# Kernel tuning notes

Hardware: AMD Instinct MI355X
Metric: run time of the kernel (lower is better)

## Reference

```python
import jax, jax.numpy as jnp
import numpy as np

L = 6          # n_layers
T = 256        # seq_len
B = 32         # batch
N = 1024       # n_features (factor_dim)
H = 16         # n_heads
HD = 64        # head_dim
PD = H * HD    # packed_dim_size == N here
FF = 4096      # dim_feedforward
EPS = 1e-5


def setup_inputs() -> dict:
    key = jax.random.key(0)
    ks = jax.random.split(key, 6)
    s = 0.02  # weight init scale (xavier-ish for these dims)
    return {
        "src": jax.random.normal(ks[0], (T, B, N), jnp.float32),
        "attn_mask": jnp.zeros((T, T), jnp.float32),  # additive mask
        "Wqkv": jax.random.normal(ks[1], (L, 3 * PD, N), jnp.float32) * s,
        "bqkv": jnp.zeros((L, 3 * PD), jnp.float32),
        "Wo": jax.random.normal(ks[2], (L, N, PD), jnp.float32) * s,
        "bo": jnp.zeros((L, N), jnp.float32),
        "ln1_g": jnp.ones((L, N), jnp.float32),
        "ln1_b": jnp.zeros((L, N), jnp.float32),
        "ln2_g": jnp.ones((L, N), jnp.float32),
        "ln2_b": jnp.zeros((L, N), jnp.float32),
        "W1": jax.random.normal(ks[3], (L, FF, N), jnp.float32) * s,
        "b1": jnp.zeros((L, FF), jnp.float32),
        "W2": jax.random.normal(ks[4], (L, N, FF), jnp.float32) * s,
        "b2": jnp.zeros((L, N), jnp.float32),
        "lnf_g": jnp.ones((N,), jnp.float32),
        "lnf_b": jnp.zeros((N,), jnp.float32),
    }


def _layer_norm(x, g, b):
    m = x.mean(-1, keepdims=True)
    v = ((x - m) ** 2).mean(-1, keepdims=True)
    return (x - m) * jax.lax.rsqrt(v + EPS) * g + b


def reference(src, attn_mask, Wqkv, bqkv, Wo, bo, ln1_g, ln1_b, ln2_g, ln2_b,
              W1, b1, W2, b2, lnf_g, lnf_b):
    inv_sqrt_hd = 1.0 / np.sqrt(HD).astype(np.float32)

    def layer(x, p):
        wqkv, bq, wo, bo_, g1, bb1n, g2, bb2n, w1, bb1, w2, bb2 = p
        # --- self-attention block (pre-norm) ---
        h = _layer_norm(x, g1, bb1n)                       # [T,B,N]
        qkv = jnp.einsum('tbn,pn->tbp', h, wqkv) + bq      # [T,B,3*PD]
        q, k, v = jnp.split(qkv, 3, axis=-1)
        q = q.reshape(T, B, H, HD) * inv_sqrt_hd
        k = k.reshape(T, B, H, HD)
        v = v.reshape(T, B, H, HD)
        scores = jnp.einsum('tbhd,sbhd->bhts', q, k) + attn_mask  # [B,H,T,T]
        probs = jax.nn.softmax(scores, axis=-1)
        o = jnp.einsum('bhts,sbhd->tbhd', probs, v).reshape(T, B, PD)
        x = x + jnp.einsum('tbp,np->tbn', o, wo) + bo_
        # --- FFN block (pre-norm) ---
        h = _layer_norm(x, g2, bb2n)
        ff = jax.nn.relu(jnp.einsum('tbn,fn->tbf', h, w1) + bb1)
        x = x + jnp.einsum('tbf,nf->tbn', ff, w2) + bb2
        return x, None

    params = (Wqkv, bqkv, Wo, bo, ln1_g, ln1_b, ln2_g, ln2_b, W1, b1, W2, b2)
    x, _ = jax.lax.scan(layer, src, params)
    return _layer_norm(x, lnf_g, lnf_b)
```

## Files before the change

### kernel.cpp

```cpp
#include <hip/hip_runtime.h>
#include <math.h>

#define TS 256
#define BS 32
#define NF 1024
#define NH 16
#define HD 64
#define PD 1024
#define FFD 4096
#define NLAYER 6
#define ROWS (TS*BS)
#define LNEPS 1e-5f

typedef unsigned int u32;
typedef __attribute__((ext_vector_type(8))) short bf16x8;
typedef __attribute__((ext_vector_type(4))) float f32x4;

__device__ __forceinline__ unsigned short f2bf(float f) {
    u32 u = __builtin_bit_cast(u32, f);
    u32 r = (u + 0x7fffu + ((u >> 16) & 1u)) >> 16;
    return (unsigned short)r;
}

__device__ __forceinline__ void async16(const void* g, void* l) {
    __builtin_amdgcn_global_load_lds(
        (const __attribute__((address_space(1))) u32*)g,
        (__attribute__((address_space(3))) u32*)l, 16, 0, 0);
}

template <int BF16OUT>
__global__ __launch_bounds__(256)
void ln_kernel(const float* __restrict__ x, void* __restrict__ y,
               const float* __restrict__ g, const float* __restrict__ b) {
    int row = blockIdx.x;
    int tid = threadIdx.x;
    const float4* xr = (const float4*)(x + (size_t)row * NF);
    float4 v = xr[tid];
    float s  = v.x + v.y + v.z + v.w;
    float ss = v.x*v.x + v.y*v.y + v.z*v.z + v.w*v.w;
    #pragma unroll
    for (int off = 32; off > 0; off >>= 1) {
        s  += __shfl_down(s,  off);
        ss += __shfl_down(ss, off);
    }
    __shared__ float ws[4], wss[4];
    int wid = tid >> 6, lane = tid & 63;
    if (lane == 0) { ws[wid] = s; wss[wid] = ss; }
    __syncthreads();
    float sum   = ws[0] + ws[1] + ws[2] + ws[3];
    float sumsq = wss[0] + wss[1] + wss[2] + wss[3];
    float mean = sum * (1.0f / NF);
    float var  = sumsq * (1.0f / NF) - mean * mean;
    float rstd = rsqrtf(var + LNEPS);
    float4 gv = ((const float4*)g)[tid];
    float4 bv = ((const float4*)b)[tid];
    float4 o;
    o.x = (v.x - mean) * rstd * gv.x + bv.x;
    o.y = (v.y - mean) * rstd * gv.y + bv.y;
    o.z = (v.z - mean) * rstd * gv.z + bv.z;
    o.w = (v.w - mean) * rstd * gv.w + bv.w;
    if (BF16OUT) {
        ushort4 ov;
        ov.x = f2bf(o.x); ov.y = f2bf(o.y); ov.z = f2bf(o.z); ov.w = f2bf(o.w);
        ((ushort4*)((unsigned short*)y + (size_t)row * NF))[tid] = ov;
    } else {
        ((float4*)((float*)y + (size_t)row * NF))[tid] = o;
    }
}

__global__ __launch_bounds__(256)
void f2bf4_kernel(const float* __restrict__ s0, const float* __restrict__ s1,
                  const float* __restrict__ s2, const float* __restrict__ s3,
                  unsigned short* __restrict__ d0, unsigned short* __restrict__ d1,
                  unsigned short* __restrict__ d2, unsigned short* __restrict__ d3,
                  int n0, int n1, int n2, int n3) {
    const float* s; unsigned short* d; int n;
    switch (blockIdx.y) {
        case 0: s = s0; d = d0; n = n0; break;
        case 1: s = s1; d = d1; n = n1; break;
        case 2: s = s2; d = d2; n = n2; break;
        default: s = s3; d = d3; n = n3; break;
    }
    int i = (blockIdx.x * 256 + threadIdx.x) * 4;
    if (i >= n) return;
    float4 v = *(const float4*)(s + i);
    ushort4 o;
    o.x = f2bf(v.x); o.y = f2bf(v.y); o.z = f2bf(v.z); o.w = f2bf(v.w);
    *(ushort4*)(d + i) = o;
}

template <int MODE, int RESID>
__global__ __launch_bounds__(256)
void gemm_mfma(const unsigned short* __restrict__ A, const unsigned short* __restrict__ B,
               const float* __restrict__ bias, const float* __restrict__ resid,
               void* __restrict__ Cout, int M, int N, int K) {
    __shared__ __align__(16) unsigned short sA0[128 * 64];
    __shared__ __align__(16) unsigned short sA1[128 * 64];
    __shared__ __align__(16) unsigned short sB0[128 * 64];
    __shared__ __align__(16) unsigned short sB1[128 * 64];
    int tid = threadIdx.x;

    int Nb = N >> 7;
    int bid = blockIdx.x;
    int group = bid / (8 * Nb);
    int rem = bid - group * (8 * Nb);
    int m0 = (group * 8 + rem / Nb) * 128;
    int n0 = (rem % Nb) * 128;

    int rB = tid >> 3;
    int c0 = (tid & 7) ^ (rB & 7);
    const unsigned short* gA[4];
    const unsigned short* gB[4];
    #pragma unroll
    for (int it = 0; it < 4; it++) {
        gA[it] = A + (size_t)(m0 + rB + 32 * it) * K + c0 * 8;
        gB[it] = B + (size_t)(n0 + rB + 32 * it) * K + c0 * 8;
    }

    int wid = tid >> 6, lane = tid & 63;
    int wm = wid >> 1, wn = wid & 1;
    int quad = lane >> 4, rl = lane & 15;

    int aoff[2][4], boff[2][4];
    #pragma unroll
    for (int ks = 0; ks < 2; ks++)
        #pragma unroll
        for (int t = 0; t < 4; t++) {
            int r = wm * 64 + t * 16 + rl;
            aoff[ks][t] = r * 64 + ((ks * 4 + quad) ^ (r & 7)) * 8;
            int rn = wn * 64 + t * 16 + rl;
            boff[ks][t] = rn * 64 + ((ks * 4 + quad) ^ (rn & 7)) * 8;
        }

    f32x4 acc[4][4] = {};

    auto stage = [&](int t, unsigned short* dA, unsigned short* dB) {
        int kt = t << 6;
        #pragma unroll
        for (int it = 0; it < 4; it++) {
            async16(gA[it] + kt, dA + (tid + 256 * it) * 8);
            async16(gB[it] + kt, dB + (tid + 256 * it) * 8);
        }
    };
    auto compute = [&](const unsigned short* pA, const unsigned short* pB) {
        #pragma unroll
        for (int ks = 0; ks < 2; ks++) {
            bf16x8 a[4], b[4];
            #pragma unroll
            for (int t = 0; t < 4; t++) {
                a[t] = *(const bf16x8*)(pA + aoff[ks][t]);
                b[t] = *(const bf16x8*)(pB + boff[ks][t]);
            }
            #pragma unroll
            for (int i = 0; i < 4; i++)
                #pragma unroll
                for (int j = 0; j < 4; j++)
                    acc[i][j] = __builtin_amdgcn_mfma_f32_16x16x32_bf16(a[i], b[j], acc[i][j], 0, 0, 0);
        }
    };

    int nT = K >> 6;
    stage(0, sA0, sB0);
    for (int t = 0; t < nT; t += 2) {
        __syncthreads();
        stage(t + 1, sA1, sB1);
        compute(sA0, sB0);
        __syncthreads();
        if (t + 2 < nT) stage(t + 2, sA0, sB0);
        compute(sA1, sB1);
    }

    float bvv[4];
    #pragma unroll
    for (int nt = 0; nt < 4; nt++) bvv[nt] = bias[n0 + wn * 64 + nt * 16 + rl];
    #pragma unroll
    for (int mt = 0; mt < 4; mt++) {
        #pragma unroll
        for (int nt = 0; nt < 4; nt++) {
            #pragma unroll
            for (int r = 0; r < 4; r++) {
                int row = m0 + wm * 64 + mt * 16 + quad * 4 + r;
                int col = n0 + wn * 64 + nt * 16 + rl;
                float v = acc[mt][nt][r] + bvv[nt];
                if (MODE == 0) {
                    if (RESID) v += resid[(size_t)row * N + col];
                    ((float*)Cout)[(size_t)row * N + col] = v;
                } else if (MODE == 1) {
                    v = fmaxf(v, 0.0f);
                    ((unsigned short*)Cout)[(size_t)row * N + col] = f2bf(v);
                } else {
                    int t = row >> 5, bb = row & 31;
                    int s = col >> 10, hh = (col >> 6) & 15, d = col & 63;
                    if (s == 0) v *= 0.125f;
                    ((unsigned short*)Cout)[((((size_t)s * BS + bb) * NH + hh) * TS + t) * HD + d] = f2bf(v);
                }
            }
        }
    }
}

template <int MODE>
__global__ __launch_bounds__(512, 2)
void gemm256(const unsigned short* __restrict__ A, const unsigned short* __restrict__ B,
             const float* __restrict__ bias, void* __restrict__ Cout,
             int M, int N, int K) {
    __shared__ __align__(16) unsigned short sA[2 * 256 * 64];
    __shared__ __align__(16) unsigned short sB[2 * 256 * 64];
    int tid = threadIdx.x;
    (void)M;

    int Nb = N >> 8;
    int nwg = gridDim.x;
    int bid = blockIdx.x;
    int wgid = (bid & 7) * (nwg >> 3) + (bid >> 3);
    int gsz = 8 * Nb;
    int group = wgid / gsz, rem = wgid - group * gsz;
    int m0 = (group * 8 + rem / Nb) << 8;
    int n0 = (rem - (rem / Nb) * Nb) << 8;

    int rr = tid >> 3;
    int cd = (tid & 7) ^ (rr & 7);
    const unsigned short* gA0 = A + (size_t)(m0 + rr) * K + cd * 8;
    const unsigned short* gB0 = B + (size_t)(n0 + rr) * K + cd * 8;
    size_t sK64 = (size_t)64 * K;

    auto stgA = [&](int buf, int h, int kt) {
        unsigned short* d = sA + buf * 16384 + h * 8192 + tid * 8;
        const unsigned short* g = gA0 + (size_t)(h * 2) * sK64 + kt;
        async16(g, d);
        async16(g + sK64, d + 4096);
    };
    auto stgB = [&](int buf, int h, int kt) {
        unsigned short* d = sB + buf * 16384 + h * 8192 + tid * 8;
        const unsigned short* g = gB0 + (size_t)(h * 2) * sK64 + kt;
        async16(g, d);
        async16(g + sK64, d + 4096);
    };

    int wid = tid >> 6, lane = tid & 63;
    int wm = wid >> 2, wn = wid & 3;
    int quad = lane >> 4, rl = lane & 15;

    int aoff[4][2], boff[4][2];
    #pragma unroll
    for (int j = 0; j < 4; ++j)
        #pragma unroll
        for (int ks = 0; ks < 2; ++ks) {
            int r = j * 32 + wm * 16 + rl;
            aoff[j][ks] = r * 64 + (((ks * 4 + quad) ^ (r & 7)) << 3);
            int rn = wn * 64 + j * 16 + rl;
            boff[j][ks] = rn * 64 + (((ks * 4 + quad) ^ (rn & 7)) << 3);
        }

    f32x4 acc[8][4] = {};
    int nT = K >> 6;

    stgA(0, 0, 0); stgB(0, 0, 0); stgA(0, 1, 0); stgB(0, 1, 0);
    if (nT > 1) {
        stgA(1, 0, 64); stgB(1, 0, 64); stgA(1, 1, 64);
        asm volatile("s_waitcnt vmcnt(6)" ::: "memory");
    } else {
        asm volatile("s_waitcnt vmcnt(0)" ::: "memory");
    }
    __builtin_amdgcn_s_barrier();
    __builtin_amdgcn_sched_barrier(0);

    bf16x8 a[4][2], b[4][2];
    for (int t = 0; t < nT; ++t) {
        int buf = t & 1;
        const unsigned short* pA = sA + buf * 16384;
        const unsigned short* pB = sB + buf * 16384;
        int kt1 = (t + 1) << 6, kt2 = (t + 2) << 6;
        int s1 = (t + 1) < nT, s2 = (t + 2) < nT;

        #pragma unroll
        for (int j = 0; j < 4; ++j) {
            a[j][0] = *(const bf16x8*)(pA + aoff[j][0]);
            a[j][1] = *(const bf16x8*)(pA + aoff[j][1]);
        }
        #pragma unroll
        for (int i = 0; i < 2; ++i) {
            b[i][0] = *(const bf16x8*)(pB + boff[i][0]);
            b[i][1] = *(const bf16x8*)(pB + boff[i][1]);
        }
        if (s1) stgB(buf ^ 1, 1, kt1);
        asm volatile("s_waitcnt lgkmcnt(8)" ::: "memory");
        __builtin_amdgcn_s_barrier();
        asm volatile("s_waitcnt lgkmcnt(0)" ::: "memory");
        __builtin_amdgcn_sched_barrier(0);
        __builtin_amdgcn_s_setprio(1);
        #pragma unroll
        for (int j = 0; j < 4; ++j)
            #pragma unroll
            for (int i = 0; i < 2; ++i) {
                acc[j][i] = __builtin_amdgcn_mfma_f32_16x16x32_bf16(a[j][0], b[i][0], acc[j][i], 0, 0, 0);
                acc[j][i] = __builtin_amdgcn_mfma_f32_16x16x32_bf16(a[j][1], b[i][1], acc[j][i], 0, 0, 0);
            }
        __builtin_amdgcn_s_setprio(0);
        __builtin_amdgcn_s_barrier();
        __builtin_amdgcn_sched_barrier(0);

        #pragma unroll
        for (int i = 2; i < 4; ++i) {
            b[i][0] = *(const bf16x8*)(pB + boff[i][0]);
            b[i][1] = *(const bf16x8*)(pB + boff[i][1]);
        }
        if (s2) stgA(buf, 0, kt2);
        __builtin_amdgcn_s_barrier();
        asm volatile("s_waitcnt lgkmcnt(0)" ::: "memory");
        __builtin_amdgcn_sched_barrier(0);
        __builtin_amdgcn_s_setprio(1);
        #pragma unroll
        for (int j = 0; j < 4; ++j)
            #pragma unroll
            for (int i = 2; i < 4; ++i) {
                acc[j][i] = __builtin_amdgcn_mfma_f32_16x16x32_bf16(a[j][0], b[i][0], acc[j][i], 0, 0, 0);
                acc[j][i] = __builtin_amdgcn_mfma_f32_16x16x32_bf16(a[j][1], b[i][1], acc[j][i], 0, 0, 0);
            }
        __builtin_amdgcn_s_setprio(0);
        __builtin_amdgcn_s_barrier();
        __builtin_amdgcn_sched_barrier(0);

        #pragma unroll
        for (int j = 0; j < 4; ++j) {
            a[j][0] = *(const bf16x8*)(pA + 8192 + aoff[j][0]);
            a[j][1] = *(const bf16x8*)(pA + 8192 + aoff[j][1]);
        }
        if (s2) stgB(buf, 0, kt2);
        __builtin_amdgcn_s_barrier();
        asm volatile("s_waitcnt lgkmcnt(0)" ::: "memory");
        __builtin_amdgcn_sched_barrier(0);
        __builtin_amdgcn_s_setprio(1);
        #pragma unroll
        for (int j = 0; j < 4; ++j)
            #pragma unroll
            for (int i = 2; i < 4; ++i) {
                acc[4 + j][i] = __builtin_amdgcn_mfma_f32_16x16x32_bf16(a[j][0], b[i][0], acc[4 + j][i], 0, 0, 0);
                acc[4 + j][i] = __builtin_amdgcn_mfma_f32_16x16x32_bf16(a[j][1], b[i][1], acc[4 + j][i], 0, 0, 0);
            }
        __builtin_amdgcn_s_setprio(0);
        __builtin_amdgcn_s_barrier();
        __builtin_amdgcn_sched_barrier(0);

        if (s2) stgA(buf, 1, kt2);
        __builtin_amdgcn_s_barrier();
        asm volatile("s_waitcnt lgkmcnt(0)" ::: "memory");
        __builtin_amdgcn_sched_barrier(0);
        __builtin_amdgcn_s_setprio(1);
        #pragma unroll
        for (int j = 0; j < 4; ++j)
            #pragma unroll
            for (int i = 0; i < 2; ++i) {
                acc[4 + j][i] = __builtin_amdgcn_mfma_f32_16x16x32_bf16(a[j][0], b[i][0], acc[4 + j][i], 0, 0, 0);
                acc[4 + j][i] = __builtin_amdgcn_mfma_f32_16x16x32_bf16(a[j][1], b[i][1], acc[4 + j][i], 0, 0, 0);
            }
        __builtin_amdgcn_s_setprio(0);
        if (s2) asm volatile("s_waitcnt vmcnt(6)" ::: "memory");
        else    asm volatile("s_waitcnt vmcnt(0)" ::: "memory");
        __builtin_amdgcn_s_barrier();
        __builtin_amdgcn_sched_barrier(0);
    }

    float bvv[4];
    #pragma unroll
    for (int ni = 0; ni < 4; ++ni) bvv[ni] = bias[n0 + wn * 64 + ni * 16 + rl];
    #pragma unroll
    for (int mi = 0; mi < 8; ++mi) {
        #pragma unroll
        for (int ni = 0; ni < 4; ++ni) {
            #pragma unroll
            for (int r = 0; r < 4; ++r) {
                int row = m0 + mi * 32 + wm * 16 + quad * 4 + r;
                int col = n0 + wn * 64 + ni * 16 + rl;
                float v = acc[mi][ni][r] + bvv[ni];
                if (MODE == 1) {
                    v = fmaxf(v, 0.0f);
                    ((unsigned short*)Cout)[(size_t)row * N + col] = f2bf(v);
                } else {
                    int tt = row >> 5, bb = row & 31;
                    int s = col >> 10, hh = (col >> 6) & 15, d = col & 63;
                    if (s == 0) v *= 0.125f;
                    ((unsigned short*)Cout)[((((size_t)s * BS + bb) * NH + hh) * TS + tt) * HD + d] = f2bf(v);
                }
            }
        }
    }
}

__global__ __launch_bounds__(256, 2)
void attn_mfma(const unsigned short* __restrict__ qkvT, const float* __restrict__ mask,
               unsigned short* __restrict__ o) {
    int bx = blockIdx.x;
    int bh = bx >> 1, half = bx & 1;
    int b = bh >> 4, h = bh & 15;
    const unsigned short* qB = qkvT + (size_t)bh * TS * HD;
    const unsigned short* kB = qB + (size_t)BS * NH * TS * HD;
    const unsigned short* vB = kB + (size_t)BS * NH * TS * HD;
    int tid = threadIdx.x, lane = tid & 63, wid = tid >> 6;
    int quad = lane >> 4, rl = lane & 15;
    int tbase = half * 128 + wid * 32;

    __shared__ __align__(16) unsigned short sKV[18432];
    __shared__ __align__(16) unsigned short sP[4][1280];

    #pragma unroll
    for (int it = 0; it < 8; it++) {
        int idx = it * 256 + tid, rrow = idx >> 3, ch = idx & 7;
        *(uint4*)(sKV + rrow * 72 + ch * 8) = *(const uint4*)(kB + (size_t)rrow * 64 + ch * 8);
    }

    bf16x8 qf[2][2];
    #pragma unroll
    for (int mt = 0; mt < 2; mt++)
        #pragma unroll
        for (int ks = 0; ks < 2; ks++)
            qf[mt][ks] = *(const bf16x8*)(qB + (size_t)(tbase + mt * 16 + rl) * 64 + ks * 32 + quad * 8);

    __syncthreads();

    f32x4 S[2][16] = {};
    #pragma unroll
    for (int nt = 0; nt < 16; nt++) {
        bf16x8 k0 = *(const bf16x8*)(sKV + (nt * 16 + rl) * 72 + quad * 8);
        bf16x8 k1 = *(const bf16x8*)(sKV + (nt * 16 + rl) * 72 + 32 + quad * 8);
        #pragma unroll
        for (int mt = 0; mt < 2; mt++) {
            S[mt][nt] = __builtin_amdgcn_mfma_f32_16x16x32_bf16(qf[mt][0], k0, S[mt][nt], 0, 0, 0);
            S[mt][nt] = __builtin_amdgcn_mfma_f32_16x16x32_bf16(qf[mt][1], k1, S[mt][nt], 0, 0, 0);
        }
    }

    float linv[2][4];
    #pragma unroll
    for (int mt = 0; mt < 2; mt++) {
        #pragma unroll
        for (int r = 0; r < 4; r++) {
            int tg = tbase + mt * 16 + quad * 4 + r;
            const float* mrow = mask + (size_t)tg * TS + rl;
            float mx = -3.0e38f;
            #pragma unroll
            for (int nt = 0; nt < 16; nt++) {
                S[mt][nt][r] += mrow[nt * 16];
                mx = fmaxf(mx, S[mt][nt][r]);
            }
            mx = fmaxf(mx, __shfl_xor(mx, 1));
            mx = fmaxf(mx, __shfl_xor(mx, 2));
            mx = fmaxf(mx, __shfl_xor(mx, 4));
            mx = fmaxf(mx, __shfl_xor(mx, 8));
            float sum = 0.0f;
            #pragma unroll
            for (int nt = 0; nt < 16; nt++) {
                float p = __expf(S[mt][nt][r] - mx);
                S[mt][nt][r] = p;
                sum += p;
            }
            sum += __shfl_xor(sum, 1);
            sum += __shfl_xor(sum, 2);
            sum += __shfl_xor(sum, 4);
            sum += __shfl_xor(sum, 8);
            linv[mt][r] = 1.0f / sum;
        }
    }

    __syncthreads();
    #pragma unroll
    for (int it = 0; it < 8; it++) {
        int idx = it * 256 + tid, srow = idx >> 3, dc = idx & 7;
        bf16x8 vv = *(const bf16x8*)(vB + (size_t)srow * 64 + dc * 8);
        #pragma unroll
        for (int j = 0; j < 8; j++)
            sKV[(dc * 8 + j) * 264 + srow] = (unsigned short)vv[j];
    }
    __syncthreads();

    f32x4 O[2][4] = {};
    unsigned short* myP = sP[wid];
    #pragma unroll
    for (int sc = 0; sc < 8; sc++) {
        #pragma unroll
        for (int mt = 0; mt < 2; mt++)
            #pragma unroll
            for (int hi = 0; hi < 2; hi++)
                #pragma unroll
                for (int r = 0; r < 4; r++)
                    myP[(mt * 16 + quad * 4 + r) * 40 + hi * 16 + rl] = f2bf(S[mt][2 * sc + hi][r]);
        bf16x8 pa[2], vf[4];
        #pragma unroll
        for (int mt = 0; mt < 2; mt++)
            pa[mt] = *(const bf16x8*)(myP + (mt * 16 + rl) * 40 + quad * 8);
        #pragma unroll
        for (int nd = 0; nd < 4; nd++)
            vf[nd] = *(const bf16x8*)(sKV + (nd * 16 + rl) * 264 + sc * 32 + quad * 8);
        #pragma unroll
        for (int mt = 0; mt < 2; mt++)
            #pragma unroll
            for (int nd = 0; nd < 4; nd++)
                O[mt][nd] = __builtin_amdgcn_mfma_f32_16x16x32_bf16(pa[mt], vf[nd], O[mt][nd], 0, 0, 0);
    }

    #pragma unroll
    for (int mt = 0; mt < 2; mt++)
        #pragma unroll
        for (int nd = 0; nd < 4; nd++)
            #pragma unroll
            for (int r = 0; r < 4; r++) {
                int tg = tbase + mt * 16 + quad * 4 + r;
                int d = nd * 16 + rl;
                o[(size_t)(tg * BS + b) * PD + h * HD + d] = f2bf(O[mt][nd][r] * linv[mt][r]);
            }
}

extern "C" void kernel_launch(void* const* d_in, const int* in_sizes, int n_in,
                              void* d_out, int out_size, void* d_ws, size_t ws_size,
                              hipStream_t stream) {
    const float* src  = (const float*)d_in[0];
    const float* mask = (const float*)d_in[1];
    const float* Wqkv = (const float*)d_in[2];
    const float* bqkv = (const float*)d_in[3];
    const float* Wo   = (const float*)d_in[4];
    const float* bo   = (const float*)d_in[5];
    const float* ln1g = (const float*)d_in[6];
    const float* ln1b = (const float*)d_in[7];
    const float* ln2g = (const float*)d_in[8];
    const float* ln2b = (const float*)d_in[9];
    const float* W1   = (const float*)d_in[10];
    const float* b1   = (const float*)d_in[11];
    const float* W2   = (const float*)d_in[12];
    const float* b2   = (const float*)d_in[13];
    const float* lnfg = (const float*)d_in[14];
    const float* lnfb = (const float*)d_in[15];

    float* x = (float*)d_out;
    char* ws = (char*)d_ws;
    unsigned short* qkvT = (unsigned short*)ws;
    unsigned short* ff   = (unsigned short*)ws;
    unsigned short* h    = (unsigned short*)(ws + 67108864);
    unsigned short* o    = (unsigned short*)(ws + 83886080);
    unsigned short* wbuf = (unsigned short*)(ws + 100663296);
    unsigned short* wq = wbuf;
    unsigned short* wo = wbuf + 3145728;
    unsigned short* w1 = wbuf + 4194304;
    unsigned short* w2 = wbuf + 8388608;

    hipMemcpyAsync(x, src, (size_t)ROWS * NF * 4, hipMemcpyDeviceToDevice, stream);

    for (int l = 0; l < NLAYER; l++) {
        const float* wqkv_l = Wqkv + (size_t)l * 3 * PD * NF;
        const float* bqkv_l = bqkv + (size_t)l * 3 * PD;
        const float* wo_l   = Wo + (size_t)l * NF * PD;
        const float* bo_l   = bo + (size_t)l * NF;
        const float* w1_l   = W1 + (size_t)l * FFD * NF;
        const float* b1_l   = b1 + (size_t)l * FFD;
        const float* w2_l   = W2 + (size_t)l * NF * FFD;
        const float* b2_l   = b2 + (size_t)l * NF;

        f2bf4_kernel<<<dim3(4096, 4), 256, 0, stream>>>(
            wqkv_l, wo_l, w1_l, w2_l, wq, wo, w1, w2,
            3 * PD * NF, NF * PD, FFD * NF, NF * FFD);
        ln_kernel<1><<<ROWS, 256, 0, stream>>>(x, h, ln1g + (size_t)l * NF, ln1b + (size_t)l * NF);
        gemm256<2><<<(ROWS / 256) * (3 * PD / 256), 512, 0, stream>>>(
            h, wq, bqkv_l, qkvT, ROWS, 3 * PD, NF);
        attn_mfma<<<BS * NH * 2, 256, 0, stream>>>(qkvT, mask, o);
        gemm_mfma<0, 1><<<(ROWS / 128) * (NF / 128), 256, 0, stream>>>(
            o, wo, bo_l, x, x, ROWS, NF, PD);
        ln_kernel<1><<<ROWS, 256, 0, stream>>>(x, h, ln2g + (size_t)l * NF, ln2b + (size_t)l * NF);
        gemm256<1><<<(ROWS / 256) * (FFD / 256), 512, 0, stream>>>(
            h, w1, b1_l, ff, ROWS, FFD, NF);
        gemm_mfma<0, 1><<<(ROWS / 128) * (NF / 128), 256, 0, stream>>>(
            ff, w2, b2_l, x, x, ROWS, NF, FFD);
    }
    ln_kernel<0><<<ROWS, 256, 0, stream>>>(x, x, lnfg, lnfb);
}
```

Before: 2.153 ms.

## Reorder GEMM inner loop by K-half instead of N-half with regrouped staging

Restructures the 4-phase inner loop of the bf16 MFMA GEMM so each phase covers a full 4x4 block of 16x16 tiles over one 32-wide K slice, instead of splitting along N with both K halves per phase. Fragment registers shrink from a[4][2]/b[4][2] to a[4]/b[4], lowering register pressure. The global-to-LDS staging schedule is regrouped to match: the next tile's second A half is prefetched in phase one and three stages are issued together in phase four. The aim is fewer live VGPRs and a better match between LDS reads and MFMA work, at the cost of more LDS fragment reloads per iteration and a different vmcnt accounting that must stay correct.

New measurement: 2.198 ms. 2.1% more time.

```diff
diff --git a/kernel.cpp b/kernel.cpp
--- a/kernel.cpp
+++ b/kernel.cpp
@@ -255,9 +255,9 @@
     f32x4 acc[8][4] = {};
     int nT = K >> 6;
 
-    stgA(0, 0, 0); stgB(0, 0, 0); stgA(0, 1, 0); stgB(0, 1, 0);
+    stgA(0, 0, 0); stgB(0, 0, 0); stgB(0, 1, 0); stgA(0, 1, 0);
     if (nT > 1) {
-        stgA(1, 0, 64); stgB(1, 0, 64); stgA(1, 1, 64);
+        stgA(1, 0, 64); stgB(1, 0, 64); stgB(1, 1, 64);
         asm volatile("s_waitcnt vmcnt(6)" ::: "memory");
     } else {
         asm volatile("s_waitcnt vmcnt(0)" ::: "memory");
@@ -265,26 +265,19 @@
     __builtin_amdgcn_s_barrier();
     __builtin_amdgcn_sched_barrier(0);
 
-    bf16x8 a[4][2], b[4][2];
     for (int t = 0; t < nT; ++t) {
         int buf = t & 1;
         const unsigned short* pA = sA + buf * 16384;
         const unsigned short* pB = sB + buf * 16384;
         int kt1 = (t + 1) << 6, kt2 = (t + 2) << 6;
         int s1 = (t + 1) < nT, s2 = (t + 2) < nT;
-
-        #pragma unroll
-        for (int j = 0; j < 4; ++j) {
-            a[j][0] = *(const bf16x8*)(pA + aoff[j][0]);
-            a[j][1] = *(const bf16x8*)(pA + aoff[j][1]);
-        }
-        #pragma unroll
-        for (int i = 0; i < 2; ++i) {
-            b[i][0] = *(const bf16x8*)(pB + boff[i][0]);
-            b[i][1] = *(const bf16x8*)(pB + boff[i][1]);
-        }
-        if (s1) stgB(buf ^ 1, 1, kt1);
-        asm volatile("s_waitcnt lgkmcnt(8)" ::: "memory");
+        bf16x8 a[4], b[4];
+
+        #pragma unroll
+        for (int j = 0; j < 4; ++j) a[j] = *(const bf16x8*)(pA + aoff[j][0]);
+        #pragma unroll
+        for (int i = 0; i < 4; ++i) b[i] = *(const bf16x8*)(pB + boff[i][0]);
+        if (s1) stgA(buf ^ 1, 1, kt1);
         __builtin_amdgcn_s_barrier();
         asm volatile("s_waitcnt lgkmcnt(0)" ::: "memory");
         __builtin_amdgcn_sched_barrier(0);
@@ -292,20 +285,14 @@
         #pragma unroll
         for (int j = 0; j < 4; ++j)
             #pragma unroll
-            for (int i = 0; i < 2; ++i) {
-                acc[j][i] = __builtin_amdgcn_mfma_f32_16x16x32_bf16(a[j][0], b[i][0], acc[j][i], 0, 0, 0);
-                acc[j][i] = __builtin_amdgcn_mfma_f32_16x16x32_bf16(a[j][1], b[i][1], acc[j][i], 0, 0, 0);
-            }
+            for (int i = 0; i < 4; ++i)
+                acc[j][i] = __builtin_amdgcn_mfma_f32_16x16x32_bf16(a[j], b[i], acc[j][i], 0, 0, 0);
         __builtin_amdgcn_s_setprio(0);
         __builtin_amdgcn_s_barrier();
         __builtin_amdgcn_sched_barrier(0);
 
         #pragma unroll
-        for (int i = 2; i < 4; ++i) {
-            b[i][0] = *(const bf16x8*)(pB + boff[i][0]);
-            b[i][1] = *(const bf16x8*)(pB + boff[i][1]);
-        }
-        if (s2) stgA(buf, 0, kt2);
+        for (int j = 0; j < 4; ++j) a[j] = *(const bf16x8*)(pA + 8192 + aoff[j][0]);
         __builtin_amdgcn_s_barrier();
         asm volatile("s_waitcnt lgkmcnt(0)" ::: "memory");
         __builtin_amdgcn_sched_barrier(0);
@@ -313,20 +300,16 @@
         #pragma unroll
         for (int j = 0; j < 4; ++j)
             #pragma unroll
-            for (int i = 2; i < 4; ++i) {
-                acc[j][i] = __builtin_amdgcn_mfma_f32_16x16x32_bf16(a[j][0], b[i][0], acc[j][i], 0, 0, 0);
-                acc[j][i] = __builtin_amdgcn_mfma_f32_16x16x32_bf16(a[j][1], b[i][1], acc[j][i], 0, 0, 0);
-            }
+            for (int i = 0; i < 4; ++i)
+                acc[4 + j][i] = __builtin_amdgcn_mfma_f32_16x16x32_bf16(a[j], b[i], acc[4 + j][i], 0, 0, 0);
         __builtin_amdgcn_s_setprio(0);
         __builtin_amdgcn_s_barrier();
         __builtin_amdgcn_sched_barrier(0);
 
         #pragma unroll
-        for (int j = 0; j < 4; ++j) {
-            a[j][0] = *(const bf16x8*)(pA + 8192 + aoff[j][0]);
-            a[j][1] = *(const bf16x8*)(pA + 8192 + aoff[j][1]);
-        }
-        if (s2) stgB(buf, 0, kt2);
+        for (int j = 0; j < 4; ++j) a[j] = *(const bf16x8*)(pA + aoff[j][1]);
+        #pragma unroll
+        for (int i = 0; i < 4; ++i) b[i] = *(const bf16x8*)(pB + boff[i][1]);
         __builtin_amdgcn_s_barrier();
         asm volatile("s_waitcnt lgkmcnt(0)" ::: "memory");
         __builtin_amdgcn_sched_barrier(0);
@@ -334,15 +317,15 @@
         #pragma unroll
         for (int j = 0; j < 4; ++j)
             #pragma unroll
-            for (int i = 2; i < 4; ++i) {
-                acc[4 + j][i] = __builtin_amdgcn_mfma_f32_16x16x32_bf16(a[j][0], b[i][0], acc[4 + j][i], 0, 0, 0);
-                acc[4 + j][i] = __builtin_amdgcn_mfma_f32_16x16x32_bf16(a[j][1], b[i][1], acc[4 + j][i], 0, 0, 0);
-            }
+            for (int i = 0; i < 4; ++i)
+                acc[j][i] = __builtin_amdgcn_mfma_f32_16x16x32_bf16(a[j], b[i], acc[j][i], 0, 0, 0);
         __builtin_amdgcn_s_setprio(0);
         __builtin_amdgcn_s_barrier();
         __builtin_amdgcn_sched_barrier(0);
 
-        if (s2) stgA(buf, 1, kt2);
+        #pragma unroll
+        for (int j = 0; j < 4; ++j) a[j] = *(const bf16x8*)(pA + 8192 + aoff[j][1]);
+        if (s2) { stgA(buf, 0, kt2); stgB(buf, 0, kt2); stgB(buf, 1, kt2); }
         __builtin_amdgcn_s_barrier();
         asm volatile("s_waitcnt lgkmcnt(0)" ::: "memory");
         __builtin_amdgcn_sched_barrier(0);
@@ -350,10 +333,8 @@
         #pragma unroll
         for (int j = 0; j < 4; ++j)
             #pragma unroll
-            for (int i = 0; i < 2; ++i) {
-                acc[4 + j][i] = __builtin_amdgcn_mfma_f32_16x16x32_bf16(a[j][0], b[i][0], acc[4 + j][i], 0, 0, 0);
-                acc[4 + j][i] = __builtin_amdgcn_mfma_f32_16x16x32_bf16(a[j][1], b[i][1], acc[4 + j][i], 0, 0, 0);
-            }
+            for (int i = 0; i < 4; ++i)
+                acc[4 + j][i] = __builtin_amdgcn_mfma_f32_16x16x32_bf16(a[j], b[i], acc[4 + j][i], 0, 0, 0);
         __builtin_amdgcn_s_setprio(0);
         if (s2) asm volatile("s_waitcnt vmcnt(6)" ::: "memory");
         else    asm volatile("s_waitcnt vmcnt(0)" ::: "memory");
```
